# Optimization experiments

Hardware: AMD Instinct MI355X
Metric: run time of the kernel (lower is better)

Reference implementation:

```python
import jax, jax.numpy as jnp
import numpy as np

N = 50000        # total nodes (2 node types x 25000)
NPER = 25000     # nodes per type
E = 600000       # edges
R = 8            # num relations
NB = 4           # num bases
IND = 256        # raw input dim per node type
HID = 128        # hidden_dim
OUT = 64         # out_dim


def setup_inputs() -> dict:
    key = jax.random.key(0)
    ks = jax.random.split(key, 24)
    s_in = 1.0 / np.sqrt(IND)
    s_h = 1.0 / np.sqrt(HID)
    d = {
        "x_paper": jax.random.normal(ks[0], (NPER, IND), jnp.float32),
        "x_author": jax.random.normal(ks[1], (NPER, IND), jnp.float32),
        "W_paper": jax.random.normal(ks[2], (IND, HID), jnp.float32) * s_in,
        "b_paper": jnp.zeros((HID,), jnp.float32),
        "W_author": jax.random.normal(ks[3], (IND, HID), jnp.float32) * s_in,
        "b_author": jnp.zeros((HID,), jnp.float32),
        "bases0": jax.random.normal(ks[4], (NB, HID, HID), jnp.float32) * s_h,
        "comp0": jax.random.normal(ks[5], (R, NB), jnp.float32) * (1.0 / np.sqrt(NB)),
        "root0": jax.random.normal(ks[6], (HID, HID), jnp.float32) * s_h,
        "bias0": jnp.zeros((HID,), jnp.float32),
        "bases1": jax.random.normal(ks[7], (NB, HID, HID), jnp.float32) * s_h,
        "comp1": jax.random.normal(ks[8], (R, NB), jnp.float32) * (1.0 / np.sqrt(NB)),
        "root1": jax.random.normal(ks[9], (HID, HID), jnp.float32) * s_h,
        "bias1": jnp.zeros((HID,), jnp.float32),
        "bases2": jax.random.normal(ks[10], (NB, HID, OUT), jnp.float32) * s_h,
        "comp2": jax.random.normal(ks[11], (R, NB), jnp.float32) * (1.0 / np.sqrt(NB)),
        "root2": jax.random.normal(ks[12], (HID, OUT), jnp.float32) * s_h,
        "bias2": jnp.zeros((OUT,), jnp.float32),
        "edge_index": jax.random.randint(ks[13], (2, E), 0, N, dtype=jnp.int64),
        "edge_type": jax.random.randint(ks[14], (E,), 0, R, dtype=jnp.int64),
    }
    return d


def rgcn_conv(x, src, dst, etype, bases, comp, root, bias):
    # weight[r] = sum_b comp[r,b] * bases[b]  -> [R, in, out]
    W = jnp.einsum('rb,bio->rio', comp, bases)
    # per-(dst node, relation) mean aggregation (PyG RGCNConv default aggr='mean')
    seg = dst * R + etype                                   # [E]
    cnt = jax.ops.segment_sum(jnp.ones((E,), x.dtype), seg, num_segments=N * R)
    norm = 1.0 / jnp.maximum(cnt, 1.0)                      # [N*R]
    msg = x[src] * norm[seg][:, None]                       # [E, in]
    agg = jax.ops.segment_sum(msg, seg, num_segments=N * R) # [N*R, in]
    agg = agg.reshape(N, R, x.shape[1])                     # [N, R, in]
    return jnp.einsum('nri,rio->no', agg, W) + x @ root + bias


def reference(x_paper, x_author, W_paper, b_paper, W_author, b_author,
              bases0, comp0, root0, bias0,
              bases1, comp1, root1, bias1,
              bases2, comp2, root2, bias2,
              edge_index, edge_type):
    # Lazy linear projections + ReLU (dropout is identity in eval mode)
    hp = jax.nn.relu(x_paper @ W_paper + b_paper)
    ha = jax.nn.relu(x_author @ W_author + b_author)
    x = jnp.concatenate([hp, ha], axis=0)                   # [N, HID]

    src, dst = edge_index[0], edge_index[1]
    x_latents = [x]

    # conv 0 (i == 0: replace)
    h = jax.nn.relu(rgcn_conv(x, src, dst, edge_type, bases0, comp0, root0, bias0))
    x_latents.append(x)
    x = h

    # conv 1 (i > 0: residual add)
    h = jax.nn.relu(rgcn_conv(x, src, dst, edge_type, bases1, comp1, root1, bias1))
    x_latents.append(x)
    x = x + h

    # final conv
    out = rgcn_conv(x, src, dst, edge_type, bases2, comp2, root2, bias2)
    return (out, x_latents)
```

## Files before the change

### kernel.cpp

```cpp
#include <hip/hip_runtime.h>
#include <stdint.h>

#define NPER  25000
#define NNODE 50000
#define NEDGE 600000
#define NREL  8
#define NBASE 4
#define INDIM 256
#define HIDD  128
#define OUTD  64
#define NSEG  (NNODE * NREL)

typedef unsigned short u16;
typedef unsigned int   u32;
typedef __attribute__((ext_vector_type(8))) __bf16          bf16x8;
typedef __attribute__((ext_vector_type(8))) unsigned short  ushort8;
typedef __attribute__((ext_vector_type(4))) float           f32x4;
typedef __attribute__((ext_vector_type(2))) float           f32x2;

__device__ __forceinline__ u16 f2b(float f) {
    union { __bf16 h; u16 u; } v; v.h = (__bf16)f; return v.u;
}
__device__ __forceinline__ bf16x8 as_bf(ushort8 u) {
    union { ushort8 a; bf16x8 b; } v; v.a = u; return v.b;
}
__device__ __forceinline__ bf16x8 cvt8(const float* p) {
    f32x4 f0 = *(const f32x4*)p;
    f32x4 f1 = *(const f32x4*)(p + 4);
    ushort8 u;
#pragma unroll
    for (int i = 0; i < 4; i++) { u[i] = f2b(f0[i]); u[i + 4] = f2b(f1[i]); }
    return as_bf(u);
}
__device__ __forceinline__ float blo(u32 v) {
    union { u32 i; float f; } u; u.i = v << 16; return u.f;
}
__device__ __forceinline__ float bhi(u32 v) {
    union { u32 i; float f; } u; u.i = v & 0xffff0000u; return u.f;
}

__device__ __forceinline__ void bsw_proj_elem(const float* __restrict__ W, u16* __restrict__ out, int idx) {
    int j    = idx & 7;
    int lane = (idx >> 3) & 63;
    int rest = idx >> 9;
    int nt   = rest & 7;
    int ks   = rest >> 3;
    int col  = nt * 16 + (lane & 15);
    int k    = ks * 32 + ((lane >> 4) << 3) + j;
    out[idx] = f2b(W[(size_t)k * 128 + col]);
}
__device__ __forceinline__ void bsw_conv_elem(const float* __restrict__ bases, const float* __restrict__ root,
                                              int ncol, u16* __restrict__ out, int idx) {
    int nt_cnt = ncol >> 4;
    int j    = idx & 7;
    int lane = (idx >> 3) & 63;
    int rest = idx >> 9;
    int nt   = rest % nt_cnt;
    int ks   = rest / nt_cnt;
    int col  = nt * 16 + (lane & 15);
    int k    = ks * 32 + ((lane >> 4) << 3) + j;
    float v = (k < 512) ? bases[(size_t)k * ncol + col] : root[(size_t)(k - 512) * ncol + col];
    out[idx] = f2b(v);
}
__global__ void build_bsw_all(const float* __restrict__ Wp, const float* __restrict__ Wa,
                              const float* __restrict__ bases0, const float* __restrict__ root0,
                              const float* __restrict__ bases1, const float* __restrict__ root1,
                              const float* __restrict__ bases2, const float* __restrict__ root2,
                              u16* __restrict__ Bswp, u16* __restrict__ Bswa,
                              u16* __restrict__ Bswc0, u16* __restrict__ Bswc1, u16* __restrict__ Bswc2) {
    int b = blockIdx.x, t = threadIdx.x;
    if (b < 128)       bsw_proj_elem(Wp, Bswp, b * 256 + t);
    else if (b < 256)  bsw_proj_elem(Wa, Bswa, (b - 128) * 256 + t);
    else if (b < 576)  bsw_conv_elem(bases0, root0, HIDD, Bswc0, (b - 256) * 256 + t);
    else if (b < 896)  bsw_conv_elem(bases1, root1, HIDD, Bswc1, (b - 576) * 256 + t);
    else               bsw_conv_elem(bases2, root2, OUTD, Bswc2, (b - 896) * 256 + t);
}

__global__ void hist_kernel(const int* __restrict__ ei, const int* __restrict__ et,
                            int* __restrict__ cnt) {
    int e = blockIdx.x * blockDim.x + threadIdx.x;
    if (e >= NEDGE) return;
    int dst = ei[NEDGE + e];
    int r   = et[e];
    atomicAdd(&cnt[dst * NREL + r], 1);
}

#define SCAN_CHUNK 1024
__global__ void scan1_kernel(int* __restrict__ data, int n, int* __restrict__ bsum) {
    __shared__ int sh[256];
    int t = threadIdx.x;
    int base = blockIdx.x * SCAN_CHUNK + t * 4;
    int v[4];
#pragma unroll
    for (int i = 0; i < 4; i++) v[i] = (base + i < n) ? data[base + i] : 0;
    int tot = v[0] + v[1] + v[2] + v[3];
    sh[t] = tot; __syncthreads();
    for (int off = 1; off < 256; off <<= 1) {
        int x = (t >= off) ? sh[t - off] : 0;
        __syncthreads();
        sh[t] += x;
        __syncthreads();
    }
    int excl = sh[t] - tot;
    if (t == 255) bsum[blockIdx.x] = sh[255];
    int run = excl;
#pragma unroll
    for (int i = 0; i < 4; i++) {
        if (base + i < n) data[base + i] = run;
        run += v[i];
    }
}

__global__ void scan2_kernel(int* __restrict__ bsum, int nb) {
    __shared__ int sh[512];
    int t = threadIdx.x;
    int v = (t < nb) ? bsum[t] : 0;
    sh[t] = v; __syncthreads();
    for (int off = 1; off < 512; off <<= 1) {
        int x = (t >= off) ? sh[t - off] : 0;
        __syncthreads();
        sh[t] += x;
        __syncthreads();
    }
    if (t < nb) bsum[t] = sh[t] - v;
}

__global__ void scan3_kernel(int* __restrict__ data, int n, const int* __restrict__ bsum,
                             int* __restrict__ fill) {
    int add = bsum[blockIdx.x];
    int base = blockIdx.x * SCAN_CHUNK + threadIdx.x * 4;
#pragma unroll
    for (int i = 0; i < 4; i++) {
        int idx = base + i;
        if (idx < n) {
            int v = data[idx] + add;
            data[idx] = v;
            if (idx < NSEG) fill[idx] = v;
        }
    }
}

__global__ void scatter_kernel(const int* __restrict__ ei, const int* __restrict__ et,
                               int* __restrict__ fill, int* __restrict__ epk) {
    int e = blockIdx.x * blockDim.x + threadIdx.x;
    if (e >= NEDGE) return;
    int src = ei[e];
    int dst = ei[NEDGE + e];
    int r   = et[e];
    int pos = atomicAdd(&fill[dst * NREL + r], 1);
    epk[pos] = src | (r << 16);
}

template<int NT, bool RELU, bool RES>
__global__ __launch_bounds__(256, 8) void fused_conv16(
    const u16* __restrict__ xbf, const float* __restrict__ comp,
    const int* __restrict__ rowptr, const int* __restrict__ epk,
    const u16* __restrict__ Bsw, const float* __restrict__ bias,
    float* __restrict__ out1, u16* __restrict__ outb,
    const float* __restrict__ resid, int ldo) {
    __shared__ u16 As[16 * 512];
    __shared__ float wtab[4][4][40];
    int tid  = threadIdx.x;
    int wv   = __builtin_amdgcn_readfirstlane(tid >> 6);
    int lane = tid & 63;
    int co   = lane * 2;
    float compv = (lane < 32) ? comp[lane] : 0.f;
    const int INV = 8 << 16;
    const u16* xco = xbf + co;

    int nbase = blockIdx.x * 16 + wv * 4;

    int p[4], e[4];
#pragma unroll
    for (int i = 0; i < 4; i++) {
        int rbase = (nbase + i) * NREL;
        if (lane < 36) {
            float w = 0.f;
            if (lane < 32) {
                int r   = lane >> 2;
                int c0  = rowptr[rbase + r], c1 = rowptr[rbase + r + 1];
                int cnt = c1 - c0;
                w = compv * ((cnt > 0) ? 1.f / (float)cnt : 0.f);
            }
            wtab[wv][i][lane] = w;
        }
        p[i] = __builtin_amdgcn_readfirstlane(rowptr[rbase]);
        e[i] = __builtin_amdgcn_readfirstlane(rowptr[rbase + 8]);
    }

#pragma unroll
    for (int i = 0; i < 4; i++) {
        int lr = wv * 4 + i;
        const char* wt = (const char*)&wtab[wv][i][0];
        f32x2 av[4];
#pragma unroll
        for (int b = 0; b < 4; b++) av[b] = (f32x2){0.f, 0.f};
        int k0[8]; u32 v0[8];
#pragma unroll
        for (int j = 0; j < 8; j++) k0[j] = (p[i] + j < e[i]) ? epk[p[i] + j] : INV;
#pragma unroll
        for (int j = 0; j < 8; j++) v0[j] = *(const u32*)(xco + ((size_t)(k0[j] & 0xffff) << 7));
        for (int pc = p[i]; pc < e[i]; pc += 8) {
            int pn = pc + 8;
            int k1[8]; u32 v1[8];
#pragma unroll
            for (int j = 0; j < 8; j++) k1[j] = (pn + j < e[i]) ? epk[pn + j] : INV;
#pragma unroll
            for (int j = 0; j < 8; j++) v1[j] = *(const u32*)(xco + ((size_t)(k1[j] & 0xffff) << 7));
#pragma unroll
            for (int j = 0; j < 8; j++) {
                f32x4 w = *(const f32x4*)(wt + (((u32)k0[j] >> 16) << 4));
                f32x2 x2; x2.x = blo(v0[j]); x2.y = bhi(v0[j]);
                av[0] += w[0] * x2;
                av[1] += w[1] * x2;
                av[2] += w[2] * x2;
                av[3] += w[3] * x2;
            }
#pragma unroll
            for (int j = 0; j < 8; j++) { k0[j] = k1[j]; v0[j] = v1[j]; }
        }
        u32 swz = (u32)(lr & 7) << 4;
        char* rowp = (char*)As + lr * 1024;
#pragma unroll
        for (int b = 0; b < 4; b++) {
            u32 pk = (u32)f2b(av[b].x) | ((u32)f2b(av[b].y) << 16);
            *(u32*)(rowp + (((u32)(b * 256 + lane * 4)) ^ swz)) = pk;
        }
    }
    __syncthreads();

    constexpr int NTW = NT / 4;
    int l15 = lane & 15, quad = lane >> 4;
    int rowbase = blockIdx.x * 16;
    int xrow = rowbase + l15;
    const u16*  bp   = Bsw + lane * 8;
    const char* arow = (const char*)As + l15 * 1024;
    u32 swz2 = (u32)(l15 & 7) << 4;
    f32x4 acc[NTW];
#pragma unroll
    for (int t = 0; t < NTW; t++) acc[t] = (f32x4){0.f, 0.f, 0.f, 0.f};
#pragma unroll
    for (int ks = 0; ks < 20; ks++) {
        bf16x8 a;
        if (ks < 16) a = *(const bf16x8*)(arow + (((u32)(ks * 64 + quad * 16)) ^ swz2));
        else         a = as_bf(*(const ushort8*)(xbf + (size_t)xrow * 128 + (ks - 16) * 32 + quad * 8));
#pragma unroll
        for (int t = 0; t < NTW; t++) {
            int nt = wv * NTW + t;
            bf16x8 b = as_bf(*(const ushort8*)(bp + ((size_t)(ks * NT + nt) << 9)));
            acc[t] = __builtin_amdgcn_mfma_f32_16x16x32_bf16(a, b, acc[t], 0, 0, 0);
        }
    }
    int orow0 = rowbase + quad * 4;
#pragma unroll
    for (int r = 0; r < 4; r++) {
        int orow = orow0 + r;
#pragma unroll
        for (int t = 0; t < NTW; t++) {
            int col = (wv * NTW + t) * 16 + l15;
            float v = acc[t][r] + bias[col];
            if (RELU) v = v > 0.f ? v : 0.f;
            if (RES)  v += resid[(size_t)orow * ldo + col];
            size_t oi = (size_t)orow * ldo + col;
            if (out1) out1[oi] = v;
            if (outb) outb[oi] = f2b(v);
        }
    }
}

template<int KMAIN, bool HASX, int NW, int MW, int NT, bool RELU, bool RES, bool AF32>
__device__ __forceinline__ void gemm_core(
    int blk, const void* __restrict__ Av, const u16* __restrict__ xq,
    const u16* __restrict__ Bsw, const float* __restrict__ bias, int M,
    float* __restrict__ out1, float* __restrict__ out2, u16* __restrict__ outb,
    const float* __restrict__ resid, int ldo) {
    constexpr int KSM = KMAIN / 32;
    constexpr int KST = KSM + (HASX ? 4 : 0);
    int tid  = threadIdx.x;
    int wave = tid >> 6, lane = tid & 63;
    int l15  = lane & 15, quad = lane >> 4;
    int rowbase = blk * (NW * MW * 16) + wave * (MW * 16);
    int rA[MW];
#pragma unroll
    for (int m = 0; m < MW; m++) {
        rA[m] = rowbase + m * 16 + l15;
        if (rA[m] > M - 1) rA[m] = M - 1;
    }
    const u16* bp = Bsw + lane * 8;
    f32x4 acc[MW][NT];
#pragma unroll
    for (int m = 0; m < MW; m++)
#pragma unroll
        for (int i = 0; i < NT; i++) acc[m][i] = (f32x4){0.f, 0.f, 0.f, 0.f};
#pragma unroll
    for (int ks = 0; ks < KST; ks++) {
        bf16x8 a[MW];
#pragma unroll
        for (int m = 0; m < MW; m++) {
            if (ks < KSM) {
                if (AF32) a[m] = cvt8((const float*)Av + (size_t)rA[m] * KMAIN + ks * 32 + quad * 8);
                else      a[m] = as_bf(*(const ushort8*)((const u16*)Av + (size_t)rA[m] * KMAIN + ks * 32 + quad * 8));
            } else {
                a[m] = as_bf(*(const ushort8*)(xq + (size_t)rA[m] * 128 + (ks - KSM) * 32 + quad * 8));
            }
        }
#pragma unroll
        for (int nt = 0; nt < NT; nt++) {
            bf16x8 b = as_bf(*(const ushort8*)(bp + ((size_t)(ks * NT + nt) << 9)));
#pragma unroll
            for (int m = 0; m < MW; m++)
                acc[m][nt] = __builtin_amdgcn_mfma_f32_16x16x32_bf16(a[m], b, acc[m][nt], 0, 0, 0);
        }
    }
#pragma unroll
    for (int m = 0; m < MW; m++) {
        int orow0 = rowbase + m * 16 + quad * 4;
#pragma unroll
        for (int r = 0; r < 4; r++) {
            int orow = orow0 + r;
            if (orow < M) {
#pragma unroll
                for (int nt = 0; nt < NT; nt++) {
                    int col = nt * 16 + l15;
                    float v = acc[m][nt][r] + bias[col];
                    if (RELU) v = v > 0.f ? v : 0.f;
                    if (RES)  v += resid[(size_t)orow * ldo + col];
                    size_t oi = (size_t)orow * ldo + col;
                    if (out1) out1[oi] = v;
                    if (out2) out2[oi] = v;
                    if (outb) outb[oi] = f2b(v);
                }
            }
        }
    }
}

__global__ __launch_bounds__(256, 2) void proj2_kernel(
    const float* __restrict__ xp, const float* __restrict__ xa,
    const u16* __restrict__ Bswp, const u16* __restrict__ Bswa,
    const float* __restrict__ bp, const float* __restrict__ ba,
    float* __restrict__ lat0, float* __restrict__ lat1, u16* __restrict__ xbf0) {
    int y = blockIdx.y;
    const float* A    = y ? xa : xp;
    const u16*   B    = y ? Bswa : Bswp;
    const float* bias = y ? ba : bp;
    size_t off = (size_t)y * NPER * HIDD;
    gemm_core<256, false, 4, 1, 8, true, false, true>(
        blockIdx.x, A, nullptr, B, bias, NPER, lat0 + off, lat1 + off, xbf0 + off, nullptr, HIDD);
}

extern "C" void kernel_launch(void* const* d_in, const int* in_sizes, int n_in,
                              void* d_out, int out_size, void* d_ws, size_t ws_size,
                              hipStream_t stream) {
    const float* x_paper  = (const float*)d_in[0];
    const float* x_author = (const float*)d_in[1];
    const float* W_paper  = (const float*)d_in[2];
    const float* b_paper  = (const float*)d_in[3];
    const float* W_author = (const float*)d_in[4];
    const float* b_author = (const float*)d_in[5];
    const float* bases0   = (const float*)d_in[6];
    const float* comp0    = (const float*)d_in[7];
    const float* root0    = (const float*)d_in[8];
    const float* bias0    = (const float*)d_in[9];
    const float* bases1   = (const float*)d_in[10];
    const float* comp1    = (const float*)d_in[11];
    const float* root1    = (const float*)d_in[12];
    const float* bias1    = (const float*)d_in[13];
    const float* bases2   = (const float*)d_in[14];
    const float* comp2    = (const float*)d_in[15];
    const float* root2    = (const float*)d_in[16];
    const float* bias2    = (const float*)d_in[17];
    const int* ei         = (const int*)d_in[18];
    const int* et         = (const int*)d_in[19];

    float* ob   = (float*)d_out;
    float* outF = ob;
    float* lat0 = ob + 3200000;
    float* lat1 = ob + 9600000;
    float* lat2 = ob + 16000000;

    char* w = (char*)d_ws;
    u16*   xbf0   = (u16*)(w + 51200000);
    u16*   xbf1   = (u16*)(w + 64000000);
    u16*   Bswc0  = (u16*)(w + 76800000);
    u16*   Bswc1  = (u16*)(w + 76963840);
    u16*   Bswc2  = (u16*)(w + 77127680);
    u16*   Bswp   = (u16*)(w + 77209600);
    u16*   Bswa   = (u16*)(w + 77275136);
    int*   rowptr = (int*)(w + 77340672);
    int*   fill   = (int*)(w + 78940736);
    int*   epk    = (int*)(w + 80540736);
    int*   bsum   = (int*)(w + 82940736);

    build_bsw_all<<<1056, 256, 0, stream>>>(W_paper, W_author, bases0, root0,
                                            bases1, root1, bases2, root2,
                                            Bswp, Bswa, Bswc0, Bswc1, Bswc2);

    proj2_kernel<<<dim3((NPER + 63) / 64, 2), 256, 0, stream>>>(
        x_paper, x_author, Bswp, Bswa, b_paper, b_author, lat0, lat1, xbf0);

    hipMemsetAsync(rowptr, 0, (NSEG + 1) * sizeof(int), stream);
    hist_kernel<<<(NEDGE + 255) / 256, 256, 0, stream>>>(ei, et, rowptr);
    int nchunk = (NSEG + 1 + SCAN_CHUNK - 1) / SCAN_CHUNK;
    scan1_kernel<<<nchunk, 256, 0, stream>>>(rowptr, NSEG + 1, bsum);
    scan2_kernel<<<1, 512, 0, stream>>>(bsum, nchunk);
    scan3_kernel<<<nchunk, 256, 0, stream>>>(rowptr, NSEG + 1, bsum, fill);
    scatter_kernel<<<(NEDGE + 255) / 256, 256, 0, stream>>>(ei, et, fill, epk);

    int ngrid = NNODE / 16;

    fused_conv16<8, true, false><<<ngrid, 256, 0, stream>>>(
        xbf0, comp0, rowptr, epk, Bswc0, bias0, lat2, xbf1, nullptr, HIDD);

    fused_conv16<8, true, true><<<ngrid, 256, 0, stream>>>(
        xbf1, comp1, rowptr, epk, Bswc1, bias1, nullptr, xbf0, lat2, HIDD);

    fused_conv16<4, false, false><<<ngrid, 256, 0, stream>>>(
        xbf0, comp2, rowptr, epk, Bswc2, bias2, outF, nullptr, nullptr, OUTD);
}
```

Measured before the change: 379.1 us.

## Merge preprocessing launches: fold memset into prep, one-pass scan, co-schedule projection with scatter

The memset is folded into the weight-swizzle prep kernel. The three-kernel scan becomes a single-pass scan in which each chunk publishes its total through flagged state words and sums the totals of earlier chunks by spinning on them. The input projection GEMM and the edge scatter are merged into one kernel whose blocks split between the two jobs, so they run concurrently. This removes several launches and serialization gaps, at the cost of a spin-wait that assumes earlier blocks make forward progress and of a lookback whose work grows with the chunk index.

```diff
diff --git a/kernel.cpp b/kernel.cpp
--- a/kernel.cpp
+++ b/kernel.cpp
@@ -10,6 +10,8 @@
 #define HIDD  128
 #define OUTD  64
 #define NSEG  (NNODE * NREL)
+#define NCHUNK ((NSEG + 1 + 1023) / 1024)
+#define RDY   0x80000000u
 
 typedef unsigned short u16;
 typedef unsigned int   u32;
@@ -62,18 +64,27 @@
     float v = (k < 512) ? bases[(size_t)k * ncol + col] : root[(size_t)(k - 512) * ncol + col];
     out[idx] = f2b(v);
 }
-__global__ void build_bsw_all(const float* __restrict__ Wp, const float* __restrict__ Wa,
-                              const float* __restrict__ bases0, const float* __restrict__ root0,
-                              const float* __restrict__ bases1, const float* __restrict__ root1,
-                              const float* __restrict__ bases2, const float* __restrict__ root2,
-                              u16* __restrict__ Bswp, u16* __restrict__ Bswa,
-                              u16* __restrict__ Bswc0, u16* __restrict__ Bswc1, u16* __restrict__ Bswc2) {
+
+__global__ __launch_bounds__(256, 8) void prep_kernel(
+    const float* __restrict__ Wp, const float* __restrict__ Wa,
+    const float* __restrict__ bases0, const float* __restrict__ root0,
+    const float* __restrict__ bases1, const float* __restrict__ root1,
+    const float* __restrict__ bases2, const float* __restrict__ root2,
+    u16* __restrict__ Bswp, u16* __restrict__ Bswa,
+    u16* __restrict__ Bswc0, u16* __restrict__ Bswc1, u16* __restrict__ Bswc2,
+    int* __restrict__ rowptr, u32* __restrict__ state) {
     int b = blockIdx.x, t = threadIdx.x;
-    if (b < 128)       bsw_proj_elem(Wp, Bswp, b * 256 + t);
-    else if (b < 256)  bsw_proj_elem(Wa, Bswa, (b - 128) * 256 + t);
-    else if (b < 576)  bsw_conv_elem(bases0, root0, HIDD, Bswc0, (b - 256) * 256 + t);
-    else if (b < 896)  bsw_conv_elem(bases1, root1, HIDD, Bswc1, (b - 576) * 256 + t);
-    else               bsw_conv_elem(bases2, root2, OUTD, Bswc2, (b - 896) * 256 + t);
+    if (b < 1056) {
+        if (b < 128)       bsw_proj_elem(Wp, Bswp, b * 256 + t);
+        else if (b < 256)  bsw_proj_elem(Wa, Bswa, (b - 128) * 256 + t);
+        else if (b < 576)  bsw_conv_elem(bases0, root0, HIDD, Bswc0, (b - 256) * 256 + t);
+        else if (b < 896)  bsw_conv_elem(bases1, root1, HIDD, Bswc1, (b - 576) * 256 + t);
+        else               bsw_conv_elem(bases2, root2, OUTD, Bswc2, (b - 896) * 256 + t);
+    }
+    int gtid  = b * 256 + t;
+    int gsize = gridDim.x * 256;
+    for (int i = gtid; i <= NSEG; i += gsize) rowptr[i] = 0;
+    for (int i = gtid; i < NCHUNK; i += gsize) state[i] = 0;
 }
 
 __global__ void hist_kernel(const int* __restrict__ ei, const int* __restrict__ et,
@@ -85,14 +96,14 @@
     atomicAdd(&cnt[dst * NREL + r], 1);
 }
 
-#define SCAN_CHUNK 1024
-__global__ void scan1_kernel(int* __restrict__ data, int n, int* __restrict__ bsum) {
+__global__ __launch_bounds__(256, 8) void scan_onepass(
+    int* __restrict__ rowptr, int* __restrict__ fill, u32* __restrict__ state) {
     __shared__ int sh[256];
-    int t = threadIdx.x;
-    int base = blockIdx.x * SCAN_CHUNK + t * 4;
+    int c = blockIdx.x, t = threadIdx.x;
+    int base = c * 1024 + t * 4;
     int v[4];
 #pragma unroll
-    for (int i = 0; i < 4; i++) v[i] = (base + i < n) ? data[base + i] : 0;
+    for (int i = 0; i < 4; i++) v[i] = (base + i <= NSEG) ? rowptr[base + i] : 0;
     int tot = v[0] + v[1] + v[2] + v[3];
     sh[t] = tot; __syncthreads();
     for (int off = 1; off < 256; off <<= 1) {
@@ -102,53 +113,139 @@
         __syncthreads();
     }
     int excl = sh[t] - tot;
-    if (t == 255) bsum[blockIdx.x] = sh[255];
-    int run = excl;
-#pragma unroll
-    for (int i = 0; i < 4; i++) {
-        if (base + i < n) data[base + i] = run;
-        run += v[i];
-    }
-}
-
-__global__ void scan2_kernel(int* __restrict__ bsum, int nb) {
-    __shared__ int sh[512];
-    int t = threadIdx.x;
-    int v = (t < nb) ? bsum[t] : 0;
-    sh[t] = v; __syncthreads();
-    for (int off = 1; off < 512; off <<= 1) {
+    if (t == 255)
+        __hip_atomic_store(&state[c], (u32)sh[255] | RDY,
+                           __ATOMIC_RELEASE, __HIP_MEMORY_SCOPE_AGENT);
+
+    int part = 0;
+    for (int i = t; i < c; i += 256) {
+        u32 s; int spins = 0;
+        for (;;) {
+            s = __hip_atomic_load(&state[i], __ATOMIC_ACQUIRE, __HIP_MEMORY_SCOPE_AGENT);
+            if (s & RDY) break;
+            __builtin_amdgcn_s_sleep(2);
+            if (++spins > (1 << 22)) break;
+        }
+        part += (int)(s & 0x7fffffffu);
+    }
+    __syncthreads();
+    sh[t] = part; __syncthreads();
+    for (int off = 1; off < 256; off <<= 1) {
         int x = (t >= off) ? sh[t - off] : 0;
         __syncthreads();
         sh[t] += x;
         __syncthreads();
     }
-    if (t < nb) bsum[t] = sh[t] - v;
-}
-
-__global__ void scan3_kernel(int* __restrict__ data, int n, const int* __restrict__ bsum,
-                             int* __restrict__ fill) {
-    int add = bsum[blockIdx.x];
-    int base = blockIdx.x * SCAN_CHUNK + threadIdx.x * 4;
+    int prefix = sh[255];
+
+    int run = excl + prefix;
 #pragma unroll
     for (int i = 0; i < 4; i++) {
         int idx = base + i;
-        if (idx < n) {
-            int v = data[idx] + add;
-            data[idx] = v;
-            if (idx < NSEG) fill[idx] = v;
-        }
-    }
-}
-
-__global__ void scatter_kernel(const int* __restrict__ ei, const int* __restrict__ et,
-                               int* __restrict__ fill, int* __restrict__ epk) {
-    int e = blockIdx.x * blockDim.x + threadIdx.x;
-    if (e >= NEDGE) return;
-    int src = ei[e];
-    int dst = ei[NEDGE + e];
-    int r   = et[e];
-    int pos = atomicAdd(&fill[dst * NREL + r], 1);
-    epk[pos] = src | (r << 16);
+        if (idx <= NSEG) {
+            rowptr[idx] = run;
+            if (idx < NSEG) fill[idx] = run;
+        }
+        run += v[i];
+    }
+}
+
+template<int KMAIN, bool HASX, int NW, int MW, int NT, bool RELU, bool RES, bool AF32>
+__device__ __forceinline__ void gemm_core(
+    int blk, const void* __restrict__ Av, const u16* __restrict__ xq,
+    const u16* __restrict__ Bsw, const float* __restrict__ bias, int M,
+    float* __restrict__ out1, float* __restrict__ out2, u16* __restrict__ outb,
+    const float* __restrict__ resid, int ldo) {
+    constexpr int KSM = KMAIN / 32;
+    constexpr int KST = KSM + (HASX ? 4 : 0);
+    int tid  = threadIdx.x;
+    int wave = tid >> 6, lane = tid & 63;
+    int l15  = lane & 15, quad = lane >> 4;
+    int rowbase = blk * (NW * MW * 16) + wave * (MW * 16);
+    int rA[MW];
+#pragma unroll
+    for (int m = 0; m < MW; m++) {
+        rA[m] = rowbase + m * 16 + l15;
+        if (rA[m] > M - 1) rA[m] = M - 1;
+    }
+    const u16* bp = Bsw + lane * 8;
+    f32x4 acc[MW][NT];
+#pragma unroll
+    for (int m = 0; m < MW; m++)
+#pragma unroll
+        for (int i = 0; i < NT; i++) acc[m][i] = (f32x4){0.f, 0.f, 0.f, 0.f};
+#pragma unroll
+    for (int ks = 0; ks < KST; ks++) {
+        bf16x8 a[MW];
+#pragma unroll
+        for (int m = 0; m < MW; m++) {
+            if (ks < KSM) {
+                if (AF32) a[m] = cvt8((const float*)Av + (size_t)rA[m] * KMAIN + ks * 32 + quad * 8);
+                else      a[m] = as_bf(*(const ushort8*)((const u16*)Av + (size_t)rA[m] * KMAIN + ks * 32 + quad * 8));
+            } else {
+                a[m] = as_bf(*(const ushort8*)(xq + (size_t)rA[m] * 128 + (ks - KSM) * 32 + quad * 8));
+            }
+        }
+#pragma unroll
+        for (int nt = 0; nt < NT; nt++) {
+            bf16x8 b = as_bf(*(const ushort8*)(bp + ((size_t)(ks * NT + nt) << 9)));
+#pragma unroll
+            for (int m = 0; m < MW; m++)
+                acc[m][nt] = __builtin_amdgcn_mfma_f32_16x16x32_bf16(a[m], b, acc[m][nt], 0, 0, 0);
+        }
+    }
+#pragma unroll
+    for (int m = 0; m < MW; m++) {
+        int orow0 = rowbase + m * 16 + quad * 4;
+#pragma unroll
+        for (int r = 0; r < 4; r++) {
+            int orow = orow0 + r;
+            if (orow < M) {
+#pragma unroll
+                for (int nt = 0; nt < NT; nt++) {
+                    int col = nt * 16 + l15;
+                    float v = acc[m][nt][r] + bias[col];
+                    if (RELU) v = v > 0.f ? v : 0.f;
+                    if (RES)  v += resid[(size_t)orow * ldo + col];
+                    size_t oi = (size_t)orow * ldo + col;
+                    if (out1) out1[oi] = v;
+                    if (out2) out2[oi] = v;
+                    if (outb) outb[oi] = f2b(v);
+                }
+            }
+        }
+    }
+}
+
+#define SPGRID 2048
+__global__ __launch_bounds__(256, 2) void sp_kernel(
+    const float* __restrict__ xp, const float* __restrict__ xa,
+    const u16* __restrict__ Bswp, const u16* __restrict__ Bswa,
+    const float* __restrict__ bp, const float* __restrict__ ba,
+    float* __restrict__ lat0, float* __restrict__ lat1, u16* __restrict__ xbf0,
+    const int* __restrict__ ei, const int* __restrict__ et,
+    int* __restrict__ fill, int* __restrict__ epk) {
+    int b = blockIdx.x;
+    if (b < 782) {
+        int y   = (b >= 391) ? 1 : 0;
+        int blk = y ? b - 391 : b;
+        const float* A    = y ? xa : xp;
+        const u16*   B    = y ? Bswa : Bswp;
+        const float* bias = y ? ba : bp;
+        size_t off = (size_t)y * NPER * HIDD;
+        gemm_core<256, false, 4, 1, 8, true, false, true>(
+            blk, A, nullptr, B, bias, NPER, lat0 + off, lat1 + off, xbf0 + off, nullptr, HIDD);
+    } else {
+        int e0 = (b - 782) * 256 + threadIdx.x;
+        const int estride = (SPGRID - 782) * 256;
+        for (int e = e0; e < NEDGE; e += estride) {
+            int src = ei[e];
+            int dst = ei[NEDGE + e];
+            int r   = et[e];
+            int pos = atomicAdd(&fill[dst * NREL + r], 1);
+            epk[pos] = src | (r << 16);
+        }
+    }
 }
 
 template<int NT, bool RELU, bool RES>
@@ -238,17 +335,17 @@
     u32 swz2 = (u32)(l15 & 7) << 4;
     f32x4 acc[NTW];
 #pragma unroll
-    for (int t = 0; t < NTW; t++) acc[t] = (f32x4){0.f, 0.f, 0.f, 0.f};
+    for (int n = 0; n < NTW; n++) acc[n] = (f32x4){0.f, 0.f, 0.f, 0.f};
 #pragma unroll
     for (int ks = 0; ks < 20; ks++) {
         bf16x8 a;
         if (ks < 16) a = *(const bf16x8*)(arow + (((u32)(ks * 64 + quad * 16)) ^ swz2));
         else         a = as_bf(*(const ushort8*)(xbf + (size_t)xrow * 128 + (ks - 16) * 32 + quad * 8));
 #pragma unroll
-        for (int t = 0; t < NTW; t++) {
-            int nt = wv * NTW + t;
+        for (int n = 0; n < NTW; n++) {
+            int nt = wv * NTW + n;
             bf16x8 b = as_bf(*(const ushort8*)(bp + ((size_t)(ks * NT + nt) << 9)));
-            acc[t] = __builtin_amdgcn_mfma_f32_16x16x32_bf16(a, b, acc[t], 0, 0, 0);
+            acc[n] = __builtin_amdgcn_mfma_f32_16x16x32_bf16(a, b, acc[n], 0, 0, 0);
         }
     }
     int orow0 = rowbase + quad * 4;
@@ -256,9 +353,9 @@
     for (int r = 0; r < 4; r++) {
         int orow = orow0 + r;
 #pragma unroll
-        for (int t = 0; t < NTW; t++) {
-            int col = (wv * NTW + t) * 16 + l15;
-            float v = acc[t][r] + bias[col];
+        for (int n = 0; n < NTW; n++) {
+            int col = (wv * NTW + n) * 16 + l15;
+            float v = acc[n][r] + bias[col];
             if (RELU) v = v > 0.f ? v : 0.f;
             if (RES)  v += resid[(size_t)orow * ldo + col];
             size_t oi = (size_t)orow * ldo + col;
@@ -266,87 +363,6 @@
             if (outb) outb[oi] = f2b(v);
         }
     }
-}
-
-template<int KMAIN, bool HASX, int NW, int MW, int NT, bool RELU, bool RES, bool AF32>
-__device__ __forceinline__ void gemm_core(
-    int blk, const void* __restrict__ Av, const u16* __restrict__ xq,
-    const u16* __restrict__ Bsw, const float* __restrict__ bias, int M,
-    float* __restrict__ out1, float* __restrict__ out2, u16* __restrict__ outb,
-    const float* __restrict__ resid, int ldo) {
-    constexpr int KSM = KMAIN / 32;
-    constexpr int KST = KSM + (HASX ? 4 : 0);
-    int tid  = threadIdx.x;
-    int wave = tid >> 6, lane = tid & 63;
-    int l15  = lane & 15, quad = lane >> 4;
-    int rowbase = blk * (NW * MW * 16) + wave * (MW * 16);
-    int rA[MW];
-#pragma unroll
-    for (int m = 0; m < MW; m++) {
-        rA[m] = rowbase + m * 16 + l15;
-        if (rA[m] > M - 1) rA[m] = M - 1;
-    }
-    const u16* bp = Bsw + lane * 8;
-    f32x4 acc[MW][NT];
-#pragma unroll
-    for (int m = 0; m < MW; m++)
-#pragma unroll
-        for (int i = 0; i < NT; i++) acc[m][i] = (f32x4){0.f, 0.f, 0.f, 0.f};
-#pragma unroll
-    for (int ks = 0; ks < KST; ks++) {
-        bf16x8 a[MW];
-#pragma unroll
-        for (int m = 0; m < MW; m++) {
-            if (ks < KSM) {
-                if (AF32) a[m] = cvt8((const float*)Av + (size_t)rA[m] * KMAIN + ks * 32 + quad * 8);
-                else      a[m] = as_bf(*(const ushort8*)((const u16*)Av + (size_t)rA[m] * KMAIN + ks * 32 + quad * 8));
-            } else {
-                a[m] = as_bf(*(const ushort8*)(xq + (size_t)rA[m] * 128 + (ks - KSM) * 32 + quad * 8));
-            }
-        }
-#pragma unroll
-        for (int nt = 0; nt < NT; nt++) {
-            bf16x8 b = as_bf(*(const ushort8*)(bp + ((size_t)(ks * NT + nt) << 9)));
-#pragma unroll
-            for (int m = 0; m < MW; m++)
-                acc[m][nt] = __builtin_amdgcn_mfma_f32_16x16x32_bf16(a[m], b, acc[m][nt], 0, 0, 0);
-        }
-    }
-#pragma unroll
-    for (int m = 0; m < MW; m++) {
-        int orow0 = rowbase + m * 16 + quad * 4;
-#pragma unroll
-        for (int r = 0; r < 4; r++) {
-            int orow = orow0 + r;
-            if (orow < M) {
-#pragma unroll
-                for (int nt = 0; nt < NT; nt++) {
-                    int col = nt * 16 + l15;
-                    float v = acc[m][nt][r] + bias[col];
-                    if (RELU) v = v > 0.f ? v : 0.f;
-                    if (RES)  v += resid[(size_t)orow * ldo + col];
-                    size_t oi = (size_t)orow * ldo + col;
-                    if (out1) out1[oi] = v;
-                    if (out2) out2[oi] = v;
-                    if (outb) outb[oi] = f2b(v);
-                }
-            }
-        }
-    }
-}
-
-__global__ __launch_bounds__(256, 2) void proj2_kernel(
-    const float* __restrict__ xp, const float* __restrict__ xa,
-    const u16* __restrict__ Bswp, const u16* __restrict__ Bswa,
-    const float* __restrict__ bp, const float* __restrict__ ba,
-    float* __restrict__ lat0, float* __restrict__ lat1, u16* __restrict__ xbf0) {
-    int y = blockIdx.y;
-    const float* A    = y ? xa : xp;
-    const u16*   B    = y ? Bswa : Bswp;
-    const float* bias = y ? ba : bp;
-    size_t off = (size_t)y * NPER * HIDD;
-    gemm_core<256, false, 4, 1, 8, true, false, true>(
-        blockIdx.x, A, nullptr, B, bias, NPER, lat0 + off, lat1 + off, xbf0 + off, nullptr, HIDD);
 }
 
 extern "C" void kernel_launch(void* const* d_in, const int* in_sizes, int n_in,
@@ -390,31 +406,25 @@
     int*   rowptr = (int*)(w + 77340672);
     int*   fill   = (int*)(w + 78940736);
     int*   epk    = (int*)(w + 80540736);
-    int*   bsum   = (int*)(w + 82940736);
-
-    build_bsw_all<<<1056, 256, 0, stream>>>(W_paper, W_author, bases0, root0,
-                                            bases1, root1, bases2, root2,
-                                            Bswp, Bswa, Bswc0, Bswc1, Bswc2);
-
-    proj2_kernel<<<dim3((NPER + 63) / 64, 2), 256, 0, stream>>>(
-        x_paper, x_author, Bswp, Bswa, b_paper, b_author, lat0, lat1, xbf0);
-
-    hipMemsetAsync(rowptr, 0, (NSEG + 1) * sizeof(int), stream);
+    u32*   state  = (u32*)(w + 82940736);
+
+    prep_kernel<<<2048, 256, 0, stream>>>(
+        W_paper, W_author, bases0, root0, bases1, root1, bases2, root2,
+        Bswp, Bswa, Bswc0, Bswc1, Bswc2, rowptr, state);
+
     hist_kernel<<<(NEDGE + 255) / 256, 256, 0, stream>>>(ei, et, rowptr);
-    int nchunk = (NSEG + 1 + SCAN_CHUNK - 1) / SCAN_CHUNK;
-    scan1_kernel<<<nchunk, 256, 0, stream>>>(rowptr, NSEG + 1, bsum);
-    scan2_kernel<<<1, 512, 0, stream>>>(bsum, nchunk);
-    scan3_kernel<<<nchunk, 256, 0, stream>>>(rowptr, NSEG + 1, bsum, fill);
-    scatter_kernel<<<(NEDGE + 255) / 256, 256, 0, stream>>>(ei, et, fill, epk);
+
+    scan_onepass<<<NCHUNK, 256, 0, stream>>>(rowptr, fill, state);
+
+    sp_kernel<<<SPGRID, 256, 0, stream>>>(
+        x_paper, x_author, Bswp, Bswa, b_paper, b_author,
+        lat0, lat1, xbf0, ei, et, fill, epk);
 
     int ngrid = NNODE / 16;
-
     fused_conv16<8, true, false><<<ngrid, 256, 0, stream>>>(
         xbf0, comp0, rowptr, epk, Bswc0, bias0, lat2, xbf1, nullptr, HIDD);
-
     fused_conv16<8, true, true><<<ngrid, 256, 0, stream>>>(
         xbf1, comp1, rowptr, epk, Bswc1, bias1, nullptr, xbf0, lat2, HIDD);
-
     fused_conv16<4, false, false><<<ngrid, 256, 0, stream>>>(
         xbf0, comp2, rowptr, epk, Bswc2, bias2, outF, nullptr, nullptr, OUTD);
 }
```

Measured after the change: 398.7 us. 1.05x slower.
